# Kernel optimization log

Measured on AMD Instinct MI355X. Metric: run time of the kernel, lower is better.

The kernel has to match this reference:

```python
import jax, jax.numpy as jnp
import numpy as np

FP8_MAX = 448.0  # max representable magnitude of float8_e4m3fn


def act_quant(x, block_size):
    """Blockwise fp8 quantization along the last dim.
    x: [M, K] -> q: [M, K//bs, bs] fp8, scale: [M, K//bs, 1] fp32."""
    m, k = x.shape
    xb = x.reshape(m, k // block_size, block_size)
    amax = jnp.max(jnp.abs(xb), axis=-1, keepdims=True)
    scale = jnp.maximum(amax, 1e-4) / FP8_MAX
    q = (xb / scale).astype(jnp.float8_e4m3fn)
    return q, scale


def dequant(q, scale):
    # q: [M, K//bs, bs], scale: [M, K//bs, 1] -> [M, K] fp32
    return (q.astype(jnp.float32) * scale).reshape(q.shape[0], -1)


def setup_inputs() -> dict:
    key = jax.random.key(0)
    k1, k2 = jax.random.split(key)
    B, S, D, F = 16, 4096, 512, 512
    x = jax.random.normal(k1, (B, S, D), dtype=jnp.float32)
    # lecun_normal-style init: std = 1/sqrt(fan_in)
    kernel = jax.random.normal(k2, (D, F), dtype=jnp.float32) / np.sqrt(D)
    bias = jnp.zeros((F,), dtype=jnp.float32)
    return {"x": x, "kernel": kernel, "bias": bias, "block_size": 128}


def reference(x, kernel, bias, block_size):
    input_shape = x.shape
    x_flat = x.reshape(-1, input_shape[-1])  # [M, K]
    # blockwise fp8 quantize activations and kernel
    xq, xs = act_quant(x_flat, block_size)
    kq, ks = act_quant(kernel, block_size)
    # fp8 GEMM with dequant scales == dequant-then-matmul in exact math
    y = dequant(xq, xs) @ dequant(kq, ks)  # [M, F]
    y = y + bias
    return y.reshape(input_shape[:-1] + (kernel.shape[1],))
```

## Files before the change

kernel.cpp:

```cpp
#include <hip/hip_runtime.h>
#include <hip/hip_bf16.h>

typedef __attribute__((ext_vector_type(4))) float  floatx4;
typedef __attribute__((ext_vector_type(2))) float  floatx2;
typedef __attribute__((ext_vector_type(8))) __bf16 bf16x8;

#define FP8_MAX 448.0f

__device__ __forceinline__ floatx2 fp8_qdq2(float a, float b) {
    int p = __builtin_amdgcn_cvt_pk_fp8_f32(a, b, 0, false);
    return __builtin_amdgcn_cvt_pk_f32_fp8(p, false);
}

__device__ __forceinline__ unsigned int f2bf(float f) {
    union { __hip_bfloat16 h; unsigned short u; } cv;
    cv.h = __float2bfloat16(f);
    return (unsigned int)cv.u;
}

__device__ __forceinline__ void async_copy16(void* lds, const void* g) {
    __builtin_amdgcn_global_load_lds(
        (const __attribute__((address_space(1))) unsigned int*)g,
        (__attribute__((address_space(3))) unsigned int*)lds, 16, 0, 0);
}

__global__ void wdq_kernel(const float* __restrict__ W,
                           __hip_bfloat16* __restrict__ Wt) {
    const int D = 512, F = 512;
    int d = blockIdx.x;
    int t = threadIdx.x;
    float4 v = *reinterpret_cast<const float4*>(W + (size_t)d * F + t * 4);
    float am = fmaxf(fmaxf(fabsf(v.x), fabsf(v.y)), fmaxf(fabsf(v.z), fabsf(v.w)));
#pragma unroll
    for (int s = 16; s >= 1; s >>= 1) am = fmaxf(am, __shfl_xor(am, s));
    float scale = fmaxf(am, 1e-4f) / FP8_MAX;
    floatx2 d01 = fp8_qdq2(v.x / scale, v.y / scale);
    floatx2 d23 = fp8_qdq2(v.z / scale, v.w / scale);
    int f0 = t * 4;
    Wt[(size_t)(f0 + 0) * D + d] = __float2bfloat16(d01[0] * scale);
    Wt[(size_t)(f0 + 1) * D + d] = __float2bfloat16(d01[1] * scale);
    Wt[(size_t)(f0 + 2) * D + d] = __float2bfloat16(d23[0] * scale);
    Wt[(size_t)(f0 + 3) * D + d] = __float2bfloat16(d23[1] * scale);
}

#define BM 64
#define BN 256

__global__ __launch_bounds__(256, 2) void fused_gemm(
        const float* __restrict__ X,
        const __hip_bfloat16* __restrict__ Wt,
        const float* __restrict__ bias,
        float* __restrict__ C, int M) {
    const int K = 512, N = 512;
    __shared__ char As[2][8192];
    __shared__ char Bs[2][32768];

    int bx = blockIdx.x, nwg = gridDim.x;
    int tile = bx;
    if ((nwg & 7) == 0) { int cpx = nwg >> 3; tile = (bx & 7) * cpx + (bx >> 3); }
    int tN = tile & 1, tM = tile >> 1;

    int tid = threadIdx.x, wid = tid >> 6, lane = tid & 63;
    int ar = tid >> 2, aq = tid & 3;

    const float* Xb = X + (size_t)tM * BM * K;
    const __hip_bfloat16* Wb = Wt + (size_t)tN * BN * K;

    float4 v[8];
    uint4  q4[4];
    floatx4 acc[4][4] = {};

    auto loadX = [&](int blk) {
        const float* src = Xb + (size_t)ar * K + blk * 128 + aq * 32;
#pragma unroll
        for (int j = 0; j < 8; ++j)
            v[j] = *reinterpret_cast<const float4*>(src + j * 4);
    };
    auto quantX = [&]() {
        float am = 0.f;
#pragma unroll
        for (int j = 0; j < 8; ++j)
            am = fmaxf(am, fmaxf(fmaxf(fabsf(v[j].x), fabsf(v[j].y)),
                                 fmaxf(fabsf(v[j].z), fabsf(v[j].w))));
        am = fmaxf(am, __shfl_xor(am, 1));
        am = fmaxf(am, __shfl_xor(am, 2));
        am = fmaxf(am, 1e-4f);
        float scale = am / FP8_MAX;
        float inv   = FP8_MAX / am;
#pragma unroll
        for (int n = 0; n < 4; ++n) {
            floatx2 a0 = fp8_qdq2(v[2*n].x*inv,   v[2*n].y*inv);
            floatx2 a1 = fp8_qdq2(v[2*n].z*inv,   v[2*n].w*inv);
            floatx2 a2 = fp8_qdq2(v[2*n+1].x*inv, v[2*n+1].y*inv);
            floatx2 a3 = fp8_qdq2(v[2*n+1].z*inv, v[2*n+1].w*inv);
            q4[n].x = f2bf(a0[0]*scale) | (f2bf(a0[1]*scale) << 16);
            q4[n].y = f2bf(a1[0]*scale) | (f2bf(a1[1]*scale) << 16);
            q4[n].z = f2bf(a2[0]*scale) | (f2bf(a2[1]*scale) << 16);
            q4[n].w = f2bf(a3[0]*scale) | (f2bf(a3[1]*scale) << 16);
        }
    };
    auto stageB = [&](int buf, int step) {
        int k0 = step * 64;
#pragma unroll
        for (int c = 0; c < 8; ++c) {
            int chunk = wid * 8 + c;
            int rr = chunk * 8 + (lane >> 3);
            int s  = lane & 7;
            const __hip_bfloat16* src =
                Wb + (size_t)rr * K + k0 + ((s ^ (rr & 7)) << 3);
            async_copy16(Bs[buf] + chunk * 1024, src);
        }
    };
    auto writeA = [&](int buf, int hb) {
        if ((aq >> 1) == hb) {
            char* base = As[buf];
#pragma unroll
            for (int n = 0; n < 4; ++n) {
                int slot = (aq & 1) * 4 + n;
                *reinterpret_cast<uint4*>(
                    base + ar * 128 + ((slot ^ (ar & 7)) << 4)) = q4[n];
            }
        }
    };
    auto mfmaStep = [&](int buf) {
        const char* ab = As[buf];
        const char* bb = Bs[buf];
#pragma unroll
        for (int ks = 0; ks < 2; ++ks) {
            int sl = ks * 4 + (lane >> 4);
            bf16x8 a[4], b[4];
#pragma unroll
            for (int mi = 0; mi < 4; ++mi) {
                int r = mi * 16 + (lane & 15);
                a[mi] = *reinterpret_cast<const bf16x8*>(
                    ab + r * 128 + ((sl ^ (r & 7)) << 4));
            }
#pragma unroll
            for (int ni = 0; ni < 4; ++ni) {
                int r = wid * 64 + ni * 16 + (lane & 15);
                b[ni] = *reinterpret_cast<const bf16x8*>(
                    bb + r * 128 + ((sl ^ (r & 7)) << 4));
            }
#pragma unroll
            for (int mi = 0; mi < 4; ++mi)
#pragma unroll
                for (int ni = 0; ni < 4; ++ni)
                    acc[mi][ni] = __builtin_amdgcn_mfma_f32_16x16x32_bf16(
                        a[mi], b[ni], acc[mi][ni], 0, 0, 0);
        }
    };

    loadX(0);
    stageB(0, 0);
    quantX();
    writeA(0, 0);
    loadX(1);
    __syncthreads();

#pragma unroll
    for (int s = 0; s < 8; ++s) {
        int cur = s & 1, nxt = cur ^ 1;
        if (s < 7) stageB(nxt, s + 1);
        if ((s & 1) == 0) {
            if (s < 7) writeA(nxt, 1);
        } else if (s < 7) {
            quantX();
            writeA(nxt, 0);
            if (s < 5) loadX((s + 3) / 2);
        }
        mfmaStep(cur);
        if (s < 7) __syncthreads();
    }

    int fcol = tN * BN + wid * 64 + (lane & 15);
    int mrow = tM * BM + ((lane >> 4) << 2);
#pragma unroll
    for (int ni = 0; ni < 4; ++ni) {
        int f = fcol + ni * 16;
        float bv = bias[f];
#pragma unroll
        for (int mi = 0; mi < 4; ++mi) {
            int m0 = mrow + mi * 16;
#pragma unroll
            for (int e = 0; e < 4; ++e)
                C[(size_t)(m0 + e) * N + f] = acc[mi][ni][e] + bv;
        }
    }
}

extern "C" void kernel_launch(void* const* d_in, const int* in_sizes, int n_in,
                              void* d_out, int out_size, void* d_ws, size_t ws_size,
                              hipStream_t stream) {
    const float* X    = (const float*)d_in[0];
    const float* W    = (const float*)d_in[1];
    const float* bias = (const float*)d_in[2];
    const int K = 512;
    const int M = in_sizes[0] / K;

    __hip_bfloat16* Wt = (__hip_bfloat16*)d_ws;

    wdq_kernel<<<dim3(512), dim3(128), 0, stream>>>(W, Wt);
    fused_gemm<<<dim3((M / BM) * (512 / BN)), dim3(256), 0, stream>>>(
        X, Wt, bias, (float*)d_out, M);
}
```

Before: 90.80 us.

## Hand-schedule GEMM pipeline with double X register buffers and explicit waitcnt barriers

Unrolls the 8-step K loop by hand and double-buffers the fp32 X loads in two register sets, so X loads are issued two steps ahead of quantization. __syncthreads is replaced with explicit vmcnt/lgkmcnt waits plus s_barrier and sched_barrier fences, and MFMA sections are wrapped in s_setprio. Bias is preloaded once before the loop. The goal is better overlap of global loads with MFMA work and less stalling at barriers, paid for with extra VGPRs that may press against the 2-waves launch bound, and fragile manual vmcnt counts.

```diff
diff --git a/kernel.cpp b/kernel.cpp
--- a/kernel.cpp
+++ b/kernel.cpp
@@ -43,9 +43,6 @@
     Wt[(size_t)(f0 + 3) * D + d] = __float2bfloat16(d23[1] * scale);
 }
 
-#define BM 64
-#define BN 256
-
 __global__ __launch_bounds__(256, 2) void fused_gemm(
         const float* __restrict__ X,
         const __hip_bfloat16* __restrict__ Wt,
@@ -55,28 +52,31 @@
     __shared__ char As[2][8192];
     __shared__ char Bs[2][32768];
 
-    int bx = blockIdx.x, nwg = gridDim.x;
-    int tile = bx;
-    if ((nwg & 7) == 0) { int cpx = nwg >> 3; tile = (bx & 7) * cpx + (bx >> 3); }
-    int tN = tile & 1, tM = tile >> 1;
+    int bx   = blockIdx.x;
+    int tile = (bx & 7) * (gridDim.x >> 3) + (bx >> 3);
+    int tN   = tile & 1;
+    int tM   = tile >> 1;
 
     int tid = threadIdx.x, wid = tid >> 6, lane = tid & 63;
+    int wn = wid;
+    int lr = lane & 15, lg = lane >> 4;
     int ar = tid >> 2, aq = tid & 3;
 
-    const float* Xb = X + (size_t)tM * BM * K;
-    const __hip_bfloat16* Wb = Wt + (size_t)tN * BN * K;
-
-    float4 v[8];
+    const float* Xb = X + (size_t)(tM * 64) * K;
+    const char* Wb  = (const char*)(Wt + (size_t)tN * 256 * K);
+    float* Cb = C + (size_t)(tM * 64) * N + tN * 256;
+
+    float4 vA[8], vB[8];
     uint4  q4[4];
     floatx4 acc[4][4] = {};
 
-    auto loadX = [&](int blk) {
-        const float* src = Xb + (size_t)ar * K + blk * 128 + aq * 32;
+    auto loadX = [&](float4 (&v)[8], int qb) {
+        const float* src = Xb + (size_t)ar * K + qb * 128 + aq * 32;
 #pragma unroll
         for (int j = 0; j < 8; ++j)
             v[j] = *reinterpret_cast<const float4*>(src + j * 4);
     };
-    auto quantX = [&]() {
+    auto quantX = [&](const float4 (&v)[8]) {
         float am = 0.f;
 #pragma unroll
         for (int j = 0; j < 8; ++j)
@@ -99,47 +99,44 @@
             q4[n].w = f2bf(a3[0]*scale) | (f2bf(a3[1]*scale) << 16);
         }
     };
-    auto stageB = [&](int buf, int step) {
-        int k0 = step * 64;
-#pragma unroll
-        for (int c = 0; c < 8; ++c) {
-            int chunk = wid * 8 + c;
-            int rr = chunk * 8 + (lane >> 3);
-            int s  = lane & 7;
-            const __hip_bfloat16* src =
-                Wb + (size_t)rr * K + k0 + ((s ^ (rr & 7)) << 3);
-            async_copy16(Bs[buf] + chunk * 1024, src);
-        }
-    };
     auto writeA = [&](int buf, int hb) {
         if ((aq >> 1) == hb) {
-            char* base = As[buf];
 #pragma unroll
             for (int n = 0; n < 4; ++n) {
                 int slot = (aq & 1) * 4 + n;
                 *reinterpret_cast<uint4*>(
-                    base + ar * 128 + ((slot ^ (ar & 7)) << 4)) = q4[n];
+                    As[buf] + ar * 128 + ((slot ^ (ar & 7)) << 4)) = q4[n];
             }
         }
     };
+    auto stageB = [&](int buf, int step) {
+        const char* base = Wb + step * 128;
+#pragma unroll
+        for (int cc = 0; cc < 8; ++cc) {
+            int c  = wid * 8 + cc;
+            int rr = c * 8 + (lane >> 3);
+            int d  = lane & 7;
+            async_copy16(Bs[buf] + c * 1024,
+                         base + (size_t)rr * (K * 2) + ((d ^ (rr & 7)) << 4));
+        }
+    };
     auto mfmaStep = [&](int buf) {
-        const char* ab = As[buf];
-        const char* bb = Bs[buf];
+        __builtin_amdgcn_s_setprio(1);
 #pragma unroll
         for (int ks = 0; ks < 2; ++ks) {
-            int sl = ks * 4 + (lane >> 4);
+            int q = (ks << 2) | lg;
             bf16x8 a[4], b[4];
 #pragma unroll
             for (int mi = 0; mi < 4; ++mi) {
-                int r = mi * 16 + (lane & 15);
+                int r = mi * 16 + lr;
                 a[mi] = *reinterpret_cast<const bf16x8*>(
-                    ab + r * 128 + ((sl ^ (r & 7)) << 4));
+                    As[buf] + r * 128 + ((q ^ (r & 7)) << 4));
             }
 #pragma unroll
             for (int ni = 0; ni < 4; ++ni) {
-                int r = wid * 64 + ni * 16 + (lane & 15);
+                int f = wn * 64 + ni * 16 + lr;
                 b[ni] = *reinterpret_cast<const bf16x8*>(
-                    bb + r * 128 + ((sl ^ (r & 7)) << 4));
+                    Bs[buf] + f * 128 + ((q ^ (f & 7)) << 4));
             }
 #pragma unroll
             for (int mi = 0; mi < 4; ++mi)
@@ -148,42 +145,81 @@
                     acc[mi][ni] = __builtin_amdgcn_mfma_f32_16x16x32_bf16(
                         a[mi], b[ni], acc[mi][ni], 0, 0, 0);
         }
-    };
-
-    loadX(0);
+        __builtin_amdgcn_s_setprio(0);
+    };
+    auto boundary = [&](int n) {
+        if (n == 8) asm volatile("s_waitcnt vmcnt(8)" ::: "memory");
+        else        asm volatile("s_waitcnt vmcnt(0)" ::: "memory");
+        asm volatile("s_waitcnt lgkmcnt(0)" ::: "memory");
+        __builtin_amdgcn_s_barrier();
+        __builtin_amdgcn_sched_barrier(0);
+    };
+
+    float bv[4];
+#pragma unroll
+    for (int ni = 0; ni < 4; ++ni)
+        bv[ni] = bias[tN * 256 + wn * 64 + ni * 16 + lr];
+    loadX(vA, 0);
+    quantX(vA);
+    writeA(0, 0);
     stageB(0, 0);
-    quantX();
-    writeA(0, 0);
-    loadX(1);
-    __syncthreads();
-
-#pragma unroll
-    for (int s = 0; s < 8; ++s) {
-        int cur = s & 1, nxt = cur ^ 1;
-        if (s < 7) stageB(nxt, s + 1);
-        if ((s & 1) == 0) {
-            if (s < 7) writeA(nxt, 1);
-        } else if (s < 7) {
-            quantX();
-            writeA(nxt, 0);
-            if (s < 5) loadX((s + 3) / 2);
-        }
-        mfmaStep(cur);
-        if (s < 7) __syncthreads();
-    }
-
-    int fcol = tN * BN + wid * 64 + (lane & 15);
-    int mrow = tM * BM + ((lane >> 4) << 2);
+    __builtin_amdgcn_sched_barrier(0);
+    loadX(vB, 1);
+    boundary(8);
+
+    stageB(1, 1);
+    __builtin_amdgcn_sched_barrier(0);
+    loadX(vA, 2);
+    writeA(1, 1);
+    mfmaStep(0);
+    boundary(8);
+
+    stageB(0, 2);
+    quantX(vB);
+    writeA(0, 0);
+    mfmaStep(1);
+    boundary(0);
+
+    stageB(1, 3);
+    __builtin_amdgcn_sched_barrier(0);
+    loadX(vB, 3);
+    writeA(1, 1);
+    mfmaStep(0);
+    boundary(8);
+
+    stageB(0, 4);
+    quantX(vA);
+    writeA(0, 0);
+    mfmaStep(1);
+    boundary(0);
+
+    stageB(1, 5);
+    writeA(1, 1);
+    mfmaStep(0);
+    boundary(0);
+
+    stageB(0, 6);
+    quantX(vB);
+    writeA(0, 0);
+    mfmaStep(1);
+    boundary(0);
+
+    stageB(1, 7);
+    writeA(1, 1);
+    mfmaStep(0);
+    boundary(0);
+
+    mfmaStep(1);
+
 #pragma unroll
     for (int ni = 0; ni < 4; ++ni) {
-        int f = fcol + ni * 16;
-        float bv = bias[f];
+        int col = wn * 64 + ni * 16 + lr;
 #pragma unroll
         for (int mi = 0; mi < 4; ++mi) {
-            int m0 = mrow + mi * 16;
+            int r0 = mi * 16 + lg * 4;
 #pragma unroll
             for (int e = 0; e < 4; ++e)
-                C[(size_t)(m0 + e) * N + f] = acc[mi][ni][e] + bv;
+                Cb[(size_t)(r0 + e) * N + col] = acc[mi][ni][e] + bv[ni];
         }
     }
 }
@@ -200,6 +236,6 @@
     __hip_bfloat16* Wt = (__hip_bfloat16*)d_ws;
 
     wdq_kernel<<<dim3(512), dim3(128), 0, stream>>>(W, Wt);
-    fused_gemm<<<dim3((M / BM) * (512 / BN)), dim3(256), 0, stream>>>(
+    fused_gemm<<<dim3((M / 64) * (512 / 256)), dim3(256), 0, stream>>>(
         X, Wt, bias, (float*)d_out, M);
 }
```

New measurement: 89.11 us. No clear change (-1.9%).

## Shrink GEMM N-tile to 128 with 2x2 wave layout and raise occupancy

Applied to the files above, without the earlier changes.

Reduces the block tile from 64x256 to 64x128, arranging the four waves in a 2x2 grid so each computes a 32x64 sub-tile. This halves B shared memory and accumulator registers, allowing three workgroups per CU and doubling the grid size. It also raises wave priority around the MFMA section. The cost is that each X tile is now loaded and quantized four times instead of twice, doubling the fp32 activation read traffic and quantization work in a kernel that is likely memory-bound.

```diff
diff --git a/kernel.cpp b/kernel.cpp
--- a/kernel.cpp
+++ b/kernel.cpp
@@ -43,35 +43,35 @@
     Wt[(size_t)(f0 + 3) * D + d] = __float2bfloat16(d23[1] * scale);
 }
 
-#define BM 64
-#define BN 256
-
-__global__ __launch_bounds__(256, 2) void fused_gemm(
+__global__ __launch_bounds__(256, 3) void fused_gemm(
         const float* __restrict__ X,
         const __hip_bfloat16* __restrict__ Wt,
         const float* __restrict__ bias,
         float* __restrict__ C, int M) {
     const int K = 512, N = 512;
     __shared__ char As[2][8192];
-    __shared__ char Bs[2][32768];
-
-    int bx = blockIdx.x, nwg = gridDim.x;
-    int tile = bx;
-    if ((nwg & 7) == 0) { int cpx = nwg >> 3; tile = (bx & 7) * cpx + (bx >> 3); }
-    int tN = tile & 1, tM = tile >> 1;
+    __shared__ char Bs[2][16384];
+
+    int bx   = blockIdx.x;
+    int tile = (bx & 7) * (gridDim.x >> 3) + (bx >> 3);
+    int tN   = tile & 3;
+    int tM   = tile >> 2;
 
     int tid = threadIdx.x, wid = tid >> 6, lane = tid & 63;
+    int wm = wid >> 1, wn = wid & 1;
+    int lr = lane & 15, lg = lane >> 4;
     int ar = tid >> 2, aq = tid & 3;
 
-    const float* Xb = X + (size_t)tM * BM * K;
-    const __hip_bfloat16* Wb = Wt + (size_t)tN * BN * K;
+    const float* Xb = X + (size_t)(tM * 64) * K;
+    const char* Wb  = (const char*)(Wt + (size_t)tN * 128 * K);
+    float* Cb = C + (size_t)(tM * 64) * N + tN * 128;
 
     float4 v[8];
     uint4  q4[4];
-    floatx4 acc[4][4] = {};
-
-    auto loadX = [&](int blk) {
-        const float* src = Xb + (size_t)ar * K + blk * 128 + aq * 32;
+    floatx4 acc[2][4] = {};
+
+    auto loadX = [&](int qb) {
+        const float* src = Xb + (size_t)ar * K + qb * 128 + aq * 32;
 #pragma unroll
         for (int j = 0; j < 8; ++j)
             v[j] = *reinterpret_cast<const float4*>(src + j * 4);
@@ -99,55 +99,53 @@
             q4[n].w = f2bf(a3[0]*scale) | (f2bf(a3[1]*scale) << 16);
         }
     };
-    auto stageB = [&](int buf, int step) {
-        int k0 = step * 64;
-#pragma unroll
-        for (int c = 0; c < 8; ++c) {
-            int chunk = wid * 8 + c;
-            int rr = chunk * 8 + (lane >> 3);
-            int s  = lane & 7;
-            const __hip_bfloat16* src =
-                Wb + (size_t)rr * K + k0 + ((s ^ (rr & 7)) << 3);
-            async_copy16(Bs[buf] + chunk * 1024, src);
-        }
-    };
     auto writeA = [&](int buf, int hb) {
         if ((aq >> 1) == hb) {
-            char* base = As[buf];
 #pragma unroll
             for (int n = 0; n < 4; ++n) {
                 int slot = (aq & 1) * 4 + n;
                 *reinterpret_cast<uint4*>(
-                    base + ar * 128 + ((slot ^ (ar & 7)) << 4)) = q4[n];
+                    As[buf] + ar * 128 + ((slot ^ (ar & 7)) << 4)) = q4[n];
             }
         }
     };
+    auto stageB = [&](int buf, int step) {
+        const char* base = Wb + step * 128;
+#pragma unroll
+        for (int cc = 0; cc < 4; ++cc) {
+            int c  = wid * 4 + cc;
+            int rr = c * 8 + (lane >> 3);
+            int d  = lane & 7;
+            async_copy16(Bs[buf] + c * 1024,
+                         base + (size_t)rr * (K * 2) + ((d ^ (rr & 7)) << 4));
+        }
+    };
     auto mfmaStep = [&](int buf) {
-        const char* ab = As[buf];
-        const char* bb = Bs[buf];
+        __builtin_amdgcn_s_setprio(1);
 #pragma unroll
         for (int ks = 0; ks < 2; ++ks) {
-            int sl = ks * 4 + (lane >> 4);
-            bf16x8 a[4], b[4];
-#pragma unroll
-            for (int mi = 0; mi < 4; ++mi) {
-                int r = mi * 16 + (lane & 15);
+            int q = (ks << 2) | lg;
+            bf16x8 a[2], b[4];
+#pragma unroll
+            for (int mi = 0; mi < 2; ++mi) {
+                int r = wm * 32 + mi * 16 + lr;
                 a[mi] = *reinterpret_cast<const bf16x8*>(
-                    ab + r * 128 + ((sl ^ (r & 7)) << 4));
+                    As[buf] + r * 128 + ((q ^ (r & 7)) << 4));
             }
 #pragma unroll
             for (int ni = 0; ni < 4; ++ni) {
-                int r = wid * 64 + ni * 16 + (lane & 15);
+                int f = wn * 64 + ni * 16 + lr;
                 b[ni] = *reinterpret_cast<const bf16x8*>(
-                    bb + r * 128 + ((sl ^ (r & 7)) << 4));
+                    Bs[buf] + f * 128 + ((q ^ (f & 7)) << 4));
             }
 #pragma unroll
-            for (int mi = 0; mi < 4; ++mi)
+            for (int mi = 0; mi < 2; ++mi)
 #pragma unroll
                 for (int ni = 0; ni < 4; ++ni)
                     acc[mi][ni] = __builtin_amdgcn_mfma_f32_16x16x32_bf16(
                         a[mi], b[ni], acc[mi][ni], 0, 0, 0);
         }
+        __builtin_amdgcn_s_setprio(0);
     };
 
     loadX(0);
@@ -172,18 +170,16 @@
         if (s < 7) __syncthreads();
     }
 
-    int fcol = tN * BN + wid * 64 + (lane & 15);
-    int mrow = tM * BM + ((lane >> 4) << 2);
 #pragma unroll
     for (int ni = 0; ni < 4; ++ni) {
-        int f = fcol + ni * 16;
-        float bv = bias[f];
-#pragma unroll
-        for (int mi = 0; mi < 4; ++mi) {
-            int m0 = mrow + mi * 16;
+        int col = wn * 64 + ni * 16 + lr;
+        float bv = bias[tN * 128 + col];
+#pragma unroll
+        for (int mi = 0; mi < 2; ++mi) {
+            int r0 = wm * 32 + mi * 16 + lg * 4;
 #pragma unroll
             for (int e = 0; e < 4; ++e)
-                C[(size_t)(m0 + e) * N + f] = acc[mi][ni][e] + bv;
+                Cb[(size_t)(r0 + e) * N + col] = acc[mi][ni][e] + bv;
         }
     }
 }
@@ -200,6 +196,6 @@
     __hip_bfloat16* Wt = (__hip_bfloat16*)d_ws;
 
     wdq_kernel<<<dim3(512), dim3(128), 0, stream>>>(W, Wt);
-    fused_gemm<<<dim3((M / BM) * (512 / BN)), dim3(256), 0, stream>>>(
+    fused_gemm<<<dim3((M / 64) * (512 / 128)), dim3(256), 0, stream>>>(
         X, Wt, bias, (float*)d_out, M);
 }
```

After: 114.9 us. 1.27x slower.
